# Optimization experiments

Hardware: AMD Instinct MI355X
Metric: run time of the kernel (lower is better)

Reference implementation:

```python
import jax, jax.numpy as jnp
import numpy as np

N_EMBD = 1024
NUM_EXPERTS = 8
TOP_K = 2


def new_gelu(x):
    # NewGELU: tanh approximation used by GPT-2
    c = jnp.sqrt(2.0 / jnp.pi).astype(x.dtype)
    return 0.5 * x * (1.0 + jnp.tanh(c * (x + 0.044715 * x ** 3)))


def setup_inputs() -> dict:
    key = jax.random.key(0)
    ks = jax.random.split(key, 6)
    C, E, H = N_EMBD, NUM_EXPERTS, 4 * N_EMBD
    x = jax.random.normal(ks[0], (4, 2048, C), dtype=jnp.float32)
    router_w = 0.02 * jax.random.normal(ks[1], (E, C), dtype=jnp.float32)  # Linear(C,E,bias=False).weight
    w1 = 0.02 * jax.random.normal(ks[2], (E, H, C), dtype=jnp.float32)     # c_fc.weight per expert
    b1 = jnp.zeros((E, H), dtype=jnp.float32)
    w2 = 0.02 * jax.random.normal(ks[3], (E, C, H), dtype=jnp.float32)     # c_proj.weight per expert
    b2 = jnp.zeros((E, C), dtype=jnp.float32)
    return {"x": x, "router_w": router_w, "w1": w1, "b1": b1, "w2": w2, "b2": b2}


def reference(x, router_w, w1, b1, w2, b2):
    B, T, C = x.shape
    E = router_w.shape[0]
    x_flat = x.reshape(B * T, C)  # [N, C]

    router_logits = x_flat @ router_w.T              # [N, E]
    router_probs = jax.nn.softmax(router_logits, axis=-1)
    top_k_probs, top_k_idx = jax.lax.top_k(router_probs, TOP_K)  # [N, K]
    top_k_probs = top_k_probs / (top_k_probs.sum(axis=-1, keepdims=True) + 1e-8)

    # combine weights per (token, expert): sum over k of gate_k * onehot(idx_k)
    cw = (jax.nn.one_hot(top_k_idx, E, dtype=x.dtype) * top_k_probs[..., None]).sum(axis=1)  # [N, E]

    output = jnp.zeros_like(x_flat)
    for e in range(E):  # small fixed expert count
        h = new_gelu(x_flat @ w1[e].T + b1[e])       # [N, 4C]
        out_e = h @ w2[e].T + b2[e]                  # [N, C]
        output = output + cw[:, e:e + 1] * out_e

    return output.reshape(B, T, C)
```

## Files before the change

kernel.cpp:

```cpp
#include <hip/hip_runtime.h>
#include <hip/hip_bf16.h>
#include <math.h>


#define N_TOK   8192
#define C_DIM   1024
#define H_DIM   4096
#define N_EXP   8
#define CAP     8192

typedef __bf16 bf16;
typedef bf16  bf16x8 __attribute__((ext_vector_type(8)));
typedef float f32x4  __attribute__((ext_vector_type(4)));

__device__ __forceinline__ void async_ld16(const void* g, void* l) {
    __builtin_amdgcn_global_load_lds(
        (const __attribute__((address_space(1))) void*)g,
        (__attribute__((address_space(3))) void*)l,
        16, 0, 0);
}

__device__ __forceinline__ float gelu_f(float v) {
    float u = v + 0.044715f * v * v * v;
    return 0.5f * v * (1.0f + tanhf(0.7978845608028654f * u));
}

#define NX8 ((size_t)N_TOK * C_DIM / 8)
#define NW8 ((size_t)N_EXP * H_DIM * C_DIM / 8)
#define NCVT (NX8 + 2 * NW8)

__global__ __launch_bounds__(256) void cvt_all_k(const float* __restrict__ x,
                                                 const float* __restrict__ w1,
                                                 const float* __restrict__ w2,
                                                 bf16* __restrict__ xb,
                                                 bf16* __restrict__ w1b,
                                                 bf16* __restrict__ w2b) {
    size_t i = (size_t)blockIdx.x * 256 + threadIdx.x;
    if (i >= NCVT) return;
    const float* src; bf16* dst; size_t j;
    if (i < NX8)            { src = x;  dst = xb;  j = i; }
    else if (i < NX8 + NW8) { src = w1; dst = w1b; j = i - NX8; }
    else                    { src = w2; dst = w2b; j = i - NX8 - NW8; }
    const float4* p = (const float4*)src + j * 2;
    float4 a = p[0], b = p[1];
    bf16x8 v;
    v[0] = (bf16)a.x; v[1] = (bf16)a.y; v[2] = (bf16)a.z; v[3] = (bf16)a.w;
    v[4] = (bf16)b.x; v[5] = (bf16)b.y; v[6] = (bf16)b.z; v[7] = (bf16)b.w;
    *((bf16x8*)dst + j) = v;
}

__global__ __launch_bounds__(1024) void router_k(const float* __restrict__ x,
                                                 const float* __restrict__ rw,
                                                 int* __restrict__ counts,
                                                 int* __restrict__ tok,
                                                 float* __restrict__ gate) {
    __shared__ int lcnt[N_EXP];
    __shared__ int lbase[N_EXP];
    const int tid  = threadIdx.x;
    const int lane = tid & 63;
    const int wv   = tid >> 6;
    if (tid < N_EXP) lcnt[tid] = 0;
    __syncthreads();

    const int t = blockIdx.x * 16 + wv;

    float dot[N_EXP];
#pragma unroll
    for (int e = 0; e < N_EXP; ++e) dot[e] = 0.f;
    const float4* xr = (const float4*)(x + (size_t)t * C_DIM);
#pragma unroll
    for (int j = 0; j < 4; ++j) {
        float4 xv = xr[j * 64 + lane];
#pragma unroll
        for (int e = 0; e < N_EXP; ++e) {
            float4 w4 = ((const float4*)(rw + (size_t)e * C_DIM))[j * 64 + lane];
            dot[e] += xv.x * w4.x + xv.y * w4.y + xv.z * w4.z + xv.w * w4.w;
        }
    }
#pragma unroll
    for (int e = 0; e < N_EXP; ++e) {
#pragma unroll
        for (int o = 32; o > 0; o >>= 1) dot[e] += __shfl_xor(dot[e], o, 64);
    }

    int a = 0, b = 0, ra = 0, rb = 0;
    float g0 = 0.f, g1 = 0.f;
    if (lane == 0) {
        float m = dot[0];
#pragma unroll
        for (int e = 1; e < N_EXP; ++e) m = fmaxf(m, dot[e]);
        float p[N_EXP]; float s = 0.f;
#pragma unroll
        for (int e = 0; e < N_EXP; ++e) { p[e] = expf(dot[e] - m); s += p[e]; }
        a = 0;
#pragma unroll
        for (int e = 1; e < N_EXP; ++e) if (p[e] > p[a]) a = e;
        b = -1;
#pragma unroll
        for (int e = 0; e < N_EXP; ++e) if (e != a && (b < 0 || p[e] > p[b])) b = e;
        float pa = p[a] / s, pb = p[b] / s;
        float d = pa + pb + 1e-8f;
        g0 = pa / d; g1 = pb / d;
        ra = atomicAdd(&lcnt[a], 1);
        rb = atomicAdd(&lcnt[b], 1);
    }
    __syncthreads();
    if (tid < N_EXP) lbase[tid] = atomicAdd(&counts[tid], lcnt[tid]);
    __syncthreads();
    if (lane == 0) {
        int sa = lbase[a] + ra;
        int sb = lbase[b] + rb;
        tok[a * CAP + sa] = t;  gate[a * CAP + sa] = g0;
        tok[b * CAP + sb] = t;  gate[b * CAP + sb] = g1;
    }
}


__global__ __launch_bounds__(256) void fc1_k(const bf16* __restrict__ xb,
                                             const bf16* __restrict__ w1b,
                                             const float* __restrict__ b1,
                                             const int* __restrict__ counts,
                                             const int* __restrict__ tok,
                                             bf16* __restrict__ h) {
    const int lin = blockIdx.x + 32 * (blockIdx.y + 64 * blockIdx.z);
    const int w   = (lin & 7) * 2048 + (lin >> 3);
    const int e   = w >> 11;
    const int by  = (w >> 5) & 63;
    const int bx  = w & 31;

    const int cnt = counts[e];
    const int m0  = by * 128;
    if (m0 >= cnt) return;
    const int n0  = bx * 128;

    int off = 0;
    for (int j = 0; j < e; ++j) off += counts[j];

    __shared__ __align__(16) bf16 As[2][128][32];
    __shared__ __align__(16) bf16 Bs[2][128][32];

    const int tid  = threadIdx.x;
    const int lane = tid & 63;
    const int wv   = tid >> 6;
    const int wm   = wv & 1;
    const int wn   = wv >> 1;

    const int scol = (((lane & 3) ^ ((lane >> 3) & 3))) * 8;

    const int ar0 = wv * 16 + (lane >> 2);
    const int ar1 = 64 + ar0;
    const int i0 = m0 + ar0, i1 = m0 + ar1;
    const int t0 = tok[e * CAP + (i0 < cnt ? i0 : cnt - 1)];
    const int t1 = tok[e * CAP + (i1 < cnt ? i1 : cnt - 1)];
    const bf16* ga0 = xb + (size_t)t0 * C_DIM + scol;
    const bf16* ga1 = xb + (size_t)t1 * C_DIM + scol;
    const bf16* gb0 = w1b + ((size_t)e * H_DIM + n0 + ar0) * C_DIM + scol;
    const bf16* gb1 = w1b + ((size_t)e * H_DIM + n0 + ar1) * C_DIM + scol;

    f32x4 acc[4][4];
#pragma unroll
    for (int mi = 0; mi < 4; ++mi)
#pragma unroll
        for (int ni = 0; ni < 4; ++ni)
#pragma unroll
            for (int r = 0; r < 4; ++r) acc[mi][ni][r] = 0.f;

    const int r_   = lane & 15;
    const int g_   = lane >> 4;
    const int rcol = (g_ ^ ((r_ >> 1) & 3)) * 8;

#define STAGE1(b, kt) do { const int k0_ = (kt) * 32;        \
    async_ld16(ga0 + k0_, &As[b][wv * 16][0]);               \
    async_ld16(ga1 + k0_, &As[b][64 + wv * 16][0]);          \
    async_ld16(gb0 + k0_, &Bs[b][wv * 16][0]);               \
    async_ld16(gb1 + k0_, &Bs[b][64 + wv * 16][0]); } while (0)

    STAGE1(0, 0);
    __syncthreads();
    int cur = 0;
    for (int kt = 0; kt < C_DIM / 32; ++kt) {
        if (kt + 1 < C_DIM / 32) STAGE1(cur ^ 1, kt + 1);

        bf16x8 af[4];
#pragma unroll
        for (int mi = 0; mi < 4; ++mi)
            af[mi] = *(const bf16x8*)&As[cur][wm * 64 + mi * 16 + r_][rcol];
#pragma unroll
        for (int ni = 0; ni < 4; ++ni) {
            bf16x8 bfr = *(const bf16x8*)&Bs[cur][wn * 64 + ni * 16 + r_][rcol];
#pragma unroll
            for (int mi = 0; mi < 4; ++mi)
                acc[mi][ni] = __builtin_amdgcn_mfma_f32_16x16x32_bf16(af[mi], bfr, acc[mi][ni], 0, 0, 0);
        }
        __syncthreads();
        cur ^= 1;
    }
#undef STAGE1

    const int lg = lane >> 4, ln = lane & 15;
#pragma unroll
    for (int mi = 0; mi < 4; ++mi) {
#pragma unroll
        for (int r = 0; r < 4; ++r) {
            const int m = wm * 64 + mi * 16 + lg * 4 + r;
            if (m0 + m < cnt) {
                const size_t hrow = (size_t)(off + m0 + m) * H_DIM;
#pragma unroll
                for (int ni = 0; ni < 4; ++ni) {
                    const int n = n0 + wn * 64 + ni * 16 + ln;
                    float v = acc[mi][ni][r] + b1[(size_t)e * H_DIM + n];
                    h[hrow + n] = (bf16)gelu_f(v);
                }
            }
        }
    }
}

__global__ __launch_bounds__(256) void fc2_k(const bf16* __restrict__ h,
                                             const bf16* __restrict__ w2b,
                                             const float* __restrict__ b2,
                                             const int* __restrict__ counts,
                                             const int* __restrict__ tok,
                                             const float* __restrict__ gate,
                                             float* __restrict__ out) {
    const int lin = blockIdx.x + 8 * (blockIdx.y + 64 * blockIdx.z);
    const int w   = (lin & 7) * 512 + (lin >> 3);
    const int e   = w >> 9;
    const int by  = (w >> 3) & 63;
    const int bx  = w & 7;

    const int cnt = counts[e];
    const int m0  = by * 128;
    if (m0 >= cnt) return;
    const int n0  = bx * 128;

    int off = 0;
    for (int j = 0; j < e; ++j) off += counts[j];

    __shared__ __align__(16) bf16 As[2][128][32];
    __shared__ __align__(16) bf16 Bs[2][128][32];

    const int tid  = threadIdx.x;
    const int lane = tid & 63;
    const int wv   = tid >> 6;
    const int wm   = wv & 1;
    const int wn   = wv >> 1;

    const int scol = (((lane & 3) ^ ((lane >> 3) & 3))) * 8;

    const int ar0 = wv * 16 + (lane >> 2);
    const int ar1 = 64 + ar0;
    const int i0 = m0 + ar0, i1 = m0 + ar1;
    const size_t hr0 = (size_t)(off + (i0 < cnt ? i0 : cnt - 1)) * H_DIM;
    const size_t hr1 = (size_t)(off + (i1 < cnt ? i1 : cnt - 1)) * H_DIM;
    const bf16* ga0 = h + hr0 + scol;
    const bf16* ga1 = h + hr1 + scol;
    const bf16* gb0 = w2b + ((size_t)e * C_DIM + n0 + ar0) * H_DIM + scol;
    const bf16* gb1 = w2b + ((size_t)e * C_DIM + n0 + ar1) * H_DIM + scol;

    f32x4 acc[4][4];
#pragma unroll
    for (int mi = 0; mi < 4; ++mi)
#pragma unroll
        for (int ni = 0; ni < 4; ++ni)
#pragma unroll
            for (int r = 0; r < 4; ++r) acc[mi][ni][r] = 0.f;

    const int r_   = lane & 15;
    const int g_   = lane >> 4;
    const int rcol = (g_ ^ ((r_ >> 1) & 3)) * 8;

#define STAGE2(b, kt) do { const int k0_ = (kt) * 32;        \
    async_ld16(ga0 + k0_, &As[b][wv * 16][0]);               \
    async_ld16(ga1 + k0_, &As[b][64 + wv * 16][0]);          \
    async_ld16(gb0 + k0_, &Bs[b][wv * 16][0]);               \
    async_ld16(gb1 + k0_, &Bs[b][64 + wv * 16][0]); } while (0)

    STAGE2(0, 0);
    __syncthreads();
    int cur = 0;
    for (int kt = 0; kt < H_DIM / 32; ++kt) {
        if (kt + 1 < H_DIM / 32) STAGE2(cur ^ 1, kt + 1);

        bf16x8 af[4];
#pragma unroll
        for (int mi = 0; mi < 4; ++mi)
            af[mi] = *(const bf16x8*)&As[cur][wm * 64 + mi * 16 + r_][rcol];
#pragma unroll
        for (int ni = 0; ni < 4; ++ni) {
            bf16x8 bfr = *(const bf16x8*)&Bs[cur][wn * 64 + ni * 16 + r_][rcol];
#pragma unroll
            for (int mi = 0; mi < 4; ++mi)
                acc[mi][ni] = __builtin_amdgcn_mfma_f32_16x16x32_bf16(af[mi], bfr, acc[mi][ni], 0, 0, 0);
        }
        __syncthreads();
        cur ^= 1;
    }
#undef STAGE2

    const int lg = lane >> 4, ln = lane & 15;
#pragma unroll
    for (int mi = 0; mi < 4; ++mi) {
#pragma unroll
        for (int r = 0; r < 4; ++r) {
            const int m = wm * 64 + mi * 16 + lg * 4 + r;
            if (m0 + m < cnt) {
                const int   tk = tok[e * CAP + m0 + m];
                const float g  = gate[e * CAP + m0 + m];
#pragma unroll
                for (int ni = 0; ni < 4; ++ni) {
                    const int n = n0 + wn * 64 + ni * 16 + ln;
                    float v = (acc[mi][ni][r] + b2[(size_t)e * C_DIM + n]) * g;
                    atomicAdd(&out[(size_t)tk * C_DIM + n], v);
                }
            }
        }
    }
}

extern "C" void kernel_launch(void* const* d_in, const int* in_sizes, int n_in,
                              void* d_out, int out_size, void* d_ws, size_t ws_size,
                              hipStream_t stream) {
    const float* x  = (const float*)d_in[0];
    const float* rw = (const float*)d_in[1];
    const float* w1 = (const float*)d_in[2];
    const float* b1 = (const float*)d_in[3];
    const float* w2 = (const float*)d_in[4];
    const float* b2 = (const float*)d_in[5];
    float* out = (float*)d_out;

    char* ws = (char*)d_ws;
    size_t o = 0;
    bf16* xb     = (bf16*)(ws + o);  o += (size_t)N_TOK * C_DIM * sizeof(bf16);
    bf16* w1b    = (bf16*)(ws + o);  o += (size_t)N_EXP * H_DIM * C_DIM * sizeof(bf16);
    bf16* w2b    = (bf16*)(ws + o);  o += (size_t)N_EXP * C_DIM * H_DIM * sizeof(bf16);
    int*  tok    = (int*)(ws + o);   o += (size_t)N_EXP * CAP * sizeof(int);
    float* gate  = (float*)(ws + o); o += (size_t)N_EXP * CAP * sizeof(float);
    int*  counts = (int*)(ws + o);   o += 128;
    bf16* h      = (bf16*)(ws + o);  o += (size_t)(2 * N_TOK) * H_DIM * sizeof(bf16);

    hipMemsetAsync(d_out, 0, (size_t)N_TOK * C_DIM * sizeof(float), stream);
    hipMemsetAsync(counts, 0, 128, stream);

    cvt_all_k<<<dim3((unsigned)((NCVT + 255) / 256)), dim3(256), 0, stream>>>(x, w1, w2, xb, w1b, w2b);
    router_k<<<dim3(N_TOK / 16), dim3(1024), 0, stream>>>(x, rw, counts, tok, gate);
    fc1_k<<<dim3(32, 64, N_EXP), dim3(256), 0, stream>>>(xb, w1b, b1, counts, tok, h);
    fc2_k<<<dim3(8, 64, N_EXP), dim3(256), 0, stream>>>(h, w2b, b2, counts, tok, gate, out);
}
```

Before: 938.9 us.

## Enlarge expert GEMM tiles to 256x256x64 with 8 waves, split-K fc2

Both expert GEMMs move from 128x128x32 tiles with 4 waves to 256x256x64 tiles with 8 waves. Each tile now stages two k-steps ahead in shared memory, controlled by explicit vmcnt waits, raw barriers and MFMA priority hints. fc2 also splits K into two halves to keep enough blocks running, and only the first half adds the bias. Larger tiles raise arithmetic intensity and cut global traffic, at the cost of more padded waste on ragged expert row counts, more registers, and twice as many atomic adds for fc2.

```diff
diff --git a/kernel.cpp b/kernel.cpp
--- a/kernel.cpp
+++ b/kernel.cpp
@@ -116,202 +116,272 @@
 }
 
 
-__global__ __launch_bounds__(256) void fc1_k(const bf16* __restrict__ xb,
-                                             const bf16* __restrict__ w1b,
-                                             const float* __restrict__ b1,
-                                             const int* __restrict__ counts,
-                                             const int* __restrict__ tok,
-                                             bf16* __restrict__ h) {
-    const int lin = blockIdx.x + 32 * (blockIdx.y + 64 * blockIdx.z);
-    const int w   = (lin & 7) * 2048 + (lin >> 3);
-    const int e   = w >> 11;
-    const int by  = (w >> 5) & 63;
-    const int bx  = w & 31;
+__global__ __launch_bounds__(512, 2) void fc1_k(const bf16* __restrict__ xb,
+                                                const bf16* __restrict__ w1b,
+                                                const float* __restrict__ b1,
+                                                const int* __restrict__ counts,
+                                                const int* __restrict__ tok,
+                                                bf16* __restrict__ h) {
+    const int lin = blockIdx.x + 16 * (blockIdx.y + 32 * blockIdx.z);
+    const int w   = (lin & 7) * 512 + (lin >> 3);
+    const int by  = w & 31;
+    const int bx  = (w >> 5) & 15;
+    const int e   = w >> 9;
 
     const int cnt = counts[e];
-    const int m0  = by * 128;
+    const int m0  = by * 256;
     if (m0 >= cnt) return;
-    const int n0  = bx * 128;
+    const int n0  = bx * 256;
 
     int off = 0;
     for (int j = 0; j < e; ++j) off += counts[j];
 
-    __shared__ __align__(16) bf16 As[2][128][32];
-    __shared__ __align__(16) bf16 Bs[2][128][32];
+    __shared__ __align__(16) bf16 As[2][256][64];
+    __shared__ __align__(16) bf16 Bs[2][256][64];
 
     const int tid  = threadIdx.x;
     const int lane = tid & 63;
     const int wv   = tid >> 6;
-    const int wm   = wv & 1;
-    const int wn   = wv >> 1;
-
-    const int scol = (((lane & 3) ^ ((lane >> 3) & 3))) * 8;
-
-    const int ar0 = wv * 16 + (lane >> 2);
-    const int ar1 = 64 + ar0;
-    const int i0 = m0 + ar0, i1 = m0 + ar1;
-    const int t0 = tok[e * CAP + (i0 < cnt ? i0 : cnt - 1)];
-    const int t1 = tok[e * CAP + (i1 < cnt ? i1 : cnt - 1)];
-    const bf16* ga0 = xb + (size_t)t0 * C_DIM + scol;
-    const bf16* ga1 = xb + (size_t)t1 * C_DIM + scol;
-    const bf16* gb0 = w1b + ((size_t)e * H_DIM + n0 + ar0) * C_DIM + scol;
-    const bf16* gb1 = w1b + ((size_t)e * H_DIM + n0 + ar1) * C_DIM + scol;
-
-    f32x4 acc[4][4];
-#pragma unroll
-    for (int mi = 0; mi < 4; ++mi)
-#pragma unroll
-        for (int ni = 0; ni < 4; ++ni)
-#pragma unroll
-            for (int r = 0; r < 4; ++r) acc[mi][ni][r] = 0.f;
-
+    const int wm   = wv >> 2;
+    const int wn   = wv & 3;
     const int r_   = lane & 15;
     const int g_   = lane >> 4;
-    const int rcol = (g_ ^ ((r_ >> 1) & 3)) * 8;
-
-#define STAGE1(b, kt) do { const int k0_ = (kt) * 32;        \
-    async_ld16(ga0 + k0_, &As[b][wv * 16][0]);               \
-    async_ld16(ga1 + k0_, &As[b][64 + wv * 16][0]);          \
-    async_ld16(gb0 + k0_, &Bs[b][wv * 16][0]);               \
-    async_ld16(gb1 + k0_, &Bs[b][64 + wv * 16][0]); } while (0)
+    const int r7   = r_ & 7;
+
+    const int row8 = tid >> 3;
+    const int col8 = (tid & 7) * 8;
+    const int scol = (((tid & 7) ^ ((tid >> 3) & 7))) * 8;
+
+    const bf16* pA[4]; const bf16* pB[4];
+#pragma unroll
+    for (int j = 0; j < 4; ++j) {
+        const int rr = j * 64 + row8;
+        const int i  = m0 + rr;
+        const int tk = tok[e * CAP + (i < cnt ? i : cnt - 1)];
+        pA[j] = xb + (size_t)tk * C_DIM + scol;
+        pB[j] = w1b + ((size_t)e * H_DIM + n0 + rr) * C_DIM + scol;
+    }
+
+    f32x4 acc[8][4];
+#pragma unroll
+    for (int mi = 0; mi < 8; ++mi)
+#pragma unroll
+        for (int ni = 0; ni < 4; ++ni)
+#pragma unroll
+            for (int r = 0; r < 4; ++r) acc[mi][ni][r] = 0.f;
+
+#define STAGE1(buf, kt) do {                                              \
+    async_ld16(pA[0] + (kt) * 64, &As[buf][  0 + row8][col8]);            \
+    async_ld16(pB[0] + (kt) * 64, &Bs[buf][  0 + row8][col8]);            \
+    async_ld16(pA[1] + (kt) * 64, &As[buf][ 64 + row8][col8]);            \
+    async_ld16(pB[1] + (kt) * 64, &Bs[buf][ 64 + row8][col8]);            \
+    async_ld16(pA[2] + (kt) * 64, &As[buf][128 + row8][col8]);            \
+    async_ld16(pB[2] + (kt) * 64, &Bs[buf][128 + row8][col8]);            \
+    async_ld16(pA[3] + (kt) * 64, &As[buf][192 + row8][col8]);            \
+    async_ld16(pB[3] + (kt) * 64, &Bs[buf][192 + row8][col8]); } while (0)
 
     STAGE1(0, 0);
-    __syncthreads();
-    int cur = 0;
-    for (int kt = 0; kt < C_DIM / 32; ++kt) {
-        if (kt + 1 < C_DIM / 32) STAGE1(cur ^ 1, kt + 1);
-
-        bf16x8 af[4];
-#pragma unroll
-        for (int mi = 0; mi < 4; ++mi)
-            af[mi] = *(const bf16x8*)&As[cur][wm * 64 + mi * 16 + r_][rcol];
-#pragma unroll
-        for (int ni = 0; ni < 4; ++ni) {
-            bf16x8 bfr = *(const bf16x8*)&Bs[cur][wn * 64 + ni * 16 + r_][rcol];
+    STAGE1(1, 1);
+    asm volatile("s_waitcnt vmcnt(8)" ::: "memory");
+    __builtin_amdgcn_sched_barrier(0);
+    __builtin_amdgcn_s_barrier();
+
+    for (int t = 0; t < C_DIM / 64; ++t) {
+        const int cur = t & 1;
+        bf16x8 bfr[4][2];
+#pragma unroll
+        for (int ni = 0; ni < 4; ++ni)
+#pragma unroll
+            for (int kk = 0; kk < 2; ++kk)
+                bfr[ni][kk] = *(const bf16x8*)&Bs[cur][wn * 64 + ni * 16 + r_][((kk * 4 + g_) ^ r7) * 8];
+
+#pragma unroll
+        for (int half = 0; half < 2; ++half) {
+            bf16x8 afr[4][2];
 #pragma unroll
             for (int mi = 0; mi < 4; ++mi)
-                acc[mi][ni] = __builtin_amdgcn_mfma_f32_16x16x32_bf16(af[mi], bfr, acc[mi][ni], 0, 0, 0);
-        }
-        __syncthreads();
-        cur ^= 1;
+#pragma unroll
+                for (int kk = 0; kk < 2; ++kk)
+                    afr[mi][kk] = *(const bf16x8*)&As[cur][wm * 128 + (half * 4 + mi) * 16 + r_][((kk * 4 + g_) ^ r7) * 8];
+            __builtin_amdgcn_s_setprio(1);
+#pragma unroll
+            for (int kk = 0; kk < 2; ++kk)
+#pragma unroll
+                for (int ni = 0; ni < 4; ++ni)
+#pragma unroll
+                    for (int mi = 0; mi < 4; ++mi)
+                        acc[half * 4 + mi][ni] = __builtin_amdgcn_mfma_f32_16x16x32_bf16(
+                            afr[mi][kk], bfr[ni][kk], acc[half * 4 + mi][ni], 0, 0, 0);
+            __builtin_amdgcn_s_setprio(0);
+        }
+        asm volatile("s_waitcnt lgkmcnt(0)" ::: "memory");
+        __builtin_amdgcn_sched_barrier(0);
+        __builtin_amdgcn_s_barrier();
+        if (t + 2 < C_DIM / 64) {
+            STAGE1(cur, t + 2);
+            asm volatile("s_waitcnt vmcnt(8)" ::: "memory");
+        } else {
+            asm volatile("s_waitcnt vmcnt(0)" ::: "memory");
+        }
+        __builtin_amdgcn_sched_barrier(0);
+        __builtin_amdgcn_s_barrier();
     }
 #undef STAGE1
 
-    const int lg = lane >> 4, ln = lane & 15;
-#pragma unroll
-    for (int mi = 0; mi < 4; ++mi) {
+    float bias[4];
+#pragma unroll
+    for (int ni = 0; ni < 4; ++ni)
+        bias[ni] = b1[(size_t)e * H_DIM + n0 + wn * 64 + ni * 16 + r_];
+
+    const int lg = lane >> 4;
+#pragma unroll
+    for (int mi = 0; mi < 8; ++mi) {
 #pragma unroll
         for (int r = 0; r < 4; ++r) {
-            const int m = wm * 64 + mi * 16 + lg * 4 + r;
+            const int m = wm * 128 + mi * 16 + lg * 4 + r;
             if (m0 + m < cnt) {
                 const size_t hrow = (size_t)(off + m0 + m) * H_DIM;
 #pragma unroll
                 for (int ni = 0; ni < 4; ++ni) {
-                    const int n = n0 + wn * 64 + ni * 16 + ln;
-                    float v = acc[mi][ni][r] + b1[(size_t)e * H_DIM + n];
-                    h[hrow + n] = (bf16)gelu_f(v);
+                    const int n = n0 + wn * 64 + ni * 16 + r_;
+                    h[hrow + n] = (bf16)gelu_f(acc[mi][ni][r] + bias[ni]);
                 }
             }
         }
     }
 }
 
-__global__ __launch_bounds__(256) void fc2_k(const bf16* __restrict__ h,
-                                             const bf16* __restrict__ w2b,
-                                             const float* __restrict__ b2,
-                                             const int* __restrict__ counts,
-                                             const int* __restrict__ tok,
-                                             const float* __restrict__ gate,
-                                             float* __restrict__ out) {
-    const int lin = blockIdx.x + 8 * (blockIdx.y + 64 * blockIdx.z);
-    const int w   = (lin & 7) * 512 + (lin >> 3);
-    const int e   = w >> 9;
-    const int by  = (w >> 3) & 63;
-    const int bx  = w & 7;
+__global__ __launch_bounds__(512, 2) void fc2_k(const bf16* __restrict__ h,
+                                                const bf16* __restrict__ w2b,
+                                                const float* __restrict__ b2,
+                                                const int* __restrict__ counts,
+                                                const int* __restrict__ tok,
+                                                const float* __restrict__ gate,
+                                                float* __restrict__ out) {
+    const int lin = blockIdx.x + 4 * (blockIdx.y + 32 * blockIdx.z);
+    const int w   = (lin & 7) * 256 + (lin >> 3);
+    const int by  = w & 31;
+    const int bx  = (w >> 5) & 3;
+    const int e   = (w >> 7) & 7;
+    const int ks  = w >> 10;
 
     const int cnt = counts[e];
-    const int m0  = by * 128;
+    const int m0  = by * 256;
     if (m0 >= cnt) return;
-    const int n0  = bx * 128;
+    const int n0  = bx * 256;
 
     int off = 0;
     for (int j = 0; j < e; ++j) off += counts[j];
 
-    __shared__ __align__(16) bf16 As[2][128][32];
-    __shared__ __align__(16) bf16 Bs[2][128][32];
+    __shared__ __align__(16) bf16 As[2][256][64];
+    __shared__ __align__(16) bf16 Bs[2][256][64];
 
     const int tid  = threadIdx.x;
     const int lane = tid & 63;
     const int wv   = tid >> 6;
-    const int wm   = wv & 1;
-    const int wn   = wv >> 1;
-
-    const int scol = (((lane & 3) ^ ((lane >> 3) & 3))) * 8;
-
-    const int ar0 = wv * 16 + (lane >> 2);
-    const int ar1 = 64 + ar0;
-    const int i0 = m0 + ar0, i1 = m0 + ar1;
-    const size_t hr0 = (size_t)(off + (i0 < cnt ? i0 : cnt - 1)) * H_DIM;
-    const size_t hr1 = (size_t)(off + (i1 < cnt ? i1 : cnt - 1)) * H_DIM;
-    const bf16* ga0 = h + hr0 + scol;
-    const bf16* ga1 = h + hr1 + scol;
-    const bf16* gb0 = w2b + ((size_t)e * C_DIM + n0 + ar0) * H_DIM + scol;
-    const bf16* gb1 = w2b + ((size_t)e * C_DIM + n0 + ar1) * H_DIM + scol;
-
-    f32x4 acc[4][4];
-#pragma unroll
-    for (int mi = 0; mi < 4; ++mi)
-#pragma unroll
-        for (int ni = 0; ni < 4; ++ni)
-#pragma unroll
-            for (int r = 0; r < 4; ++r) acc[mi][ni][r] = 0.f;
-
+    const int wm   = wv >> 2;
+    const int wn   = wv & 3;
     const int r_   = lane & 15;
     const int g_   = lane >> 4;
-    const int rcol = (g_ ^ ((r_ >> 1) & 3)) * 8;
-
-#define STAGE2(b, kt) do { const int k0_ = (kt) * 32;        \
-    async_ld16(ga0 + k0_, &As[b][wv * 16][0]);               \
-    async_ld16(ga1 + k0_, &As[b][64 + wv * 16][0]);          \
-    async_ld16(gb0 + k0_, &Bs[b][wv * 16][0]);               \
-    async_ld16(gb1 + k0_, &Bs[b][64 + wv * 16][0]); } while (0)
+    const int r7   = r_ & 7;
+
+    const int row8 = tid >> 3;
+    const int col8 = (tid & 7) * 8;
+    const int scol = (((tid & 7) ^ ((tid >> 3) & 7))) * 8;
+
+    const bf16* pA[4]; const bf16* pB[4];
+#pragma unroll
+    for (int j = 0; j < 4; ++j) {
+        const int rr = j * 64 + row8;
+        const int i  = m0 + rr;
+        pA[j] = h + (size_t)(off + (i < cnt ? i : cnt - 1)) * H_DIM + (size_t)ks * 2048 + scol;
+        pB[j] = w2b + ((size_t)e * C_DIM + n0 + rr) * H_DIM + (size_t)ks * 2048 + scol;
+    }
+
+    f32x4 acc[8][4];
+#pragma unroll
+    for (int mi = 0; mi < 8; ++mi)
+#pragma unroll
+        for (int ni = 0; ni < 4; ++ni)
+#pragma unroll
+            for (int r = 0; r < 4; ++r) acc[mi][ni][r] = 0.f;
+
+#define STAGE2(buf, kt) do {                                              \
+    async_ld16(pA[0] + (kt) * 64, &As[buf][  0 + row8][col8]);            \
+    async_ld16(pB[0] + (kt) * 64, &Bs[buf][  0 + row8][col8]);            \
+    async_ld16(pA[1] + (kt) * 64, &As[buf][ 64 + row8][col8]);            \
+    async_ld16(pB[1] + (kt) * 64, &Bs[buf][ 64 + row8][col8]);            \
+    async_ld16(pA[2] + (kt) * 64, &As[buf][128 + row8][col8]);            \
+    async_ld16(pB[2] + (kt) * 64, &Bs[buf][128 + row8][col8]);            \
+    async_ld16(pA[3] + (kt) * 64, &As[buf][192 + row8][col8]);            \
+    async_ld16(pB[3] + (kt) * 64, &Bs[buf][192 + row8][col8]); } while (0)
 
     STAGE2(0, 0);
-    __syncthreads();
-    int cur = 0;
-    for (int kt = 0; kt < H_DIM / 32; ++kt) {
-        if (kt + 1 < H_DIM / 32) STAGE2(cur ^ 1, kt + 1);
-
-        bf16x8 af[4];
-#pragma unroll
-        for (int mi = 0; mi < 4; ++mi)
-            af[mi] = *(const bf16x8*)&As[cur][wm * 64 + mi * 16 + r_][rcol];
-#pragma unroll
-        for (int ni = 0; ni < 4; ++ni) {
-            bf16x8 bfr = *(const bf16x8*)&Bs[cur][wn * 64 + ni * 16 + r_][rcol];
+    STAGE2(1, 1);
+    asm volatile("s_waitcnt vmcnt(8)" ::: "memory");
+    __builtin_amdgcn_sched_barrier(0);
+    __builtin_amdgcn_s_barrier();
+
+    for (int t = 0; t < 32; ++t) {
+        const int cur = t & 1;
+        bf16x8 bfr[4][2];
+#pragma unroll
+        for (int ni = 0; ni < 4; ++ni)
+#pragma unroll
+            for (int kk = 0; kk < 2; ++kk)
+                bfr[ni][kk] = *(const bf16x8*)&Bs[cur][wn * 64 + ni * 16 + r_][((kk * 4 + g_) ^ r7) * 8];
+
+#pragma unroll
+        for (int half = 0; half < 2; ++half) {
+            bf16x8 afr[4][2];
 #pragma unroll
             for (int mi = 0; mi < 4; ++mi)
-                acc[mi][ni] = __builtin_amdgcn_mfma_f32_16x16x32_bf16(af[mi], bfr, acc[mi][ni], 0, 0, 0);
-        }
-        __syncthreads();
-        cur ^= 1;
+#pragma unroll
+                for (int kk = 0; kk < 2; ++kk)
+                    afr[mi][kk] = *(const bf16x8*)&As[cur][wm * 128 + (half * 4 + mi) * 16 + r_][((kk * 4 + g_) ^ r7) * 8];
+            __builtin_amdgcn_s_setprio(1);
+#pragma unroll
+            for (int kk = 0; kk < 2; ++kk)
+#pragma unroll
+                for (int ni = 0; ni < 4; ++ni)
+#pragma unroll
+                    for (int mi = 0; mi < 4; ++mi)
+                        acc[half * 4 + mi][ni] = __builtin_amdgcn_mfma_f32_16x16x32_bf16(
+                            afr[mi][kk], bfr[ni][kk], acc[half * 4 + mi][ni], 0, 0, 0);
+            __builtin_amdgcn_s_setprio(0);
+        }
+        asm volatile("s_waitcnt lgkmcnt(0)" ::: "memory");
+        __builtin_amdgcn_sched_barrier(0);
+        __builtin_amdgcn_s_barrier();
+        if (t + 2 < 32) {
+            STAGE2(cur, t + 2);
+            asm volatile("s_waitcnt vmcnt(8)" ::: "memory");
+        } else {
+            asm volatile("s_waitcnt vmcnt(0)" ::: "memory");
+        }
+        __builtin_amdgcn_sched_barrier(0);
+        __builtin_amdgcn_s_barrier();
     }
 #undef STAGE2
 
-    const int lg = lane >> 4, ln = lane & 15;
-#pragma unroll
-    for (int mi = 0; mi < 4; ++mi) {
+    float bias[4];
+#pragma unroll
+    for (int ni = 0; ni < 4; ++ni)
+        bias[ni] = (ks == 0) ? b2[(size_t)e * C_DIM + n0 + wn * 64 + ni * 16 + r_] : 0.f;
+
+    const int lg = lane >> 4;
+#pragma unroll
+    for (int mi = 0; mi < 8; ++mi) {
 #pragma unroll
         for (int r = 0; r < 4; ++r) {
-            const int m = wm * 64 + mi * 16 + lg * 4 + r;
+            const int m = wm * 128 + mi * 16 + lg * 4 + r;
             if (m0 + m < cnt) {
                 const int   tk = tok[e * CAP + m0 + m];
                 const float g  = gate[e * CAP + m0 + m];
 #pragma unroll
                 for (int ni = 0; ni < 4; ++ni) {
-                    const int n = n0 + wn * 64 + ni * 16 + ln;
-                    float v = (acc[mi][ni][r] + b2[(size_t)e * C_DIM + n]) * g;
-                    atomicAdd(&out[(size_t)tk * C_DIM + n], v);
+                    const int n = n0 + wn * 64 + ni * 16 + r_;
+                    atomicAdd(&out[(size_t)tk * C_DIM + n], (acc[mi][ni][r] + bias[ni]) * g);
                 }
             }
         }
@@ -344,6 +414,6 @@
 
     cvt_all_k<<<dim3((unsigned)((NCVT + 255) / 256)), dim3(256), 0, stream>>>(x, w1, w2, xb, w1b, w2b);
     router_k<<<dim3(N_TOK / 16), dim3(1024), 0, stream>>>(x, rw, counts, tok, gate);
-    fc1_k<<<dim3(32, 64, N_EXP), dim3(256), 0, stream>>>(xb, w1b, b1, counts, tok, h);
-    fc2_k<<<dim3(8, 64, N_EXP), dim3(256), 0, stream>>>(h, w2b, b2, counts, tok, gate, out);
-}
+    fc1_k<<<dim3(16, 32, N_EXP), dim3(512), 0, stream>>>(xb, w1b, b1, counts, tok, h);
+    fc2_k<<<dim3(4, 32, 2 * N_EXP), dim3(512), 0, stream>>>(h, w2b, b2, counts, tok, gate, out);
+}
```

After: 976.8 us. +4.0%, slower.
